# Kernel tuning notes

Measured on AMD Instinct MI355X. Metric: run time of the kernel, lower is better.

The kernel has to match this reference:

```python
import jax, jax.numpy as jnp
import numpy as np

N = 100000
E = 600000
IN_DIM, HID_DIM, OUT_DIM = 128, 64, 3


def setup_inputs() -> dict:
    key = jax.random.key(0)
    ks = jax.random.split(key, 8)
    x = jax.random.normal(ks[0], (N, IN_DIM), dtype=jnp.float32)
    edge_index = jax.random.randint(ks[1], (2, E), 0, N, dtype=jnp.int64)
    # SAGEConv layer 1: lin_l (neighbors, with bias), lin_r (root, no bias)
    s1 = 1.0 / np.sqrt(IN_DIM)
    Wl1 = jax.random.uniform(ks[2], (IN_DIM, HID_DIM), jnp.float32, -s1, s1)
    Wr1 = jax.random.uniform(ks[3], (IN_DIM, HID_DIM), jnp.float32, -s1, s1)
    b1 = jnp.zeros((HID_DIM,), jnp.float32)
    # SAGEConv layer 2
    s2 = 1.0 / np.sqrt(HID_DIM)
    Wl2 = jax.random.uniform(ks[4], (HID_DIM, OUT_DIM), jnp.float32, -s2, s2)
    Wr2 = jax.random.uniform(ks[5], (HID_DIM, OUT_DIM), jnp.float32, -s2, s2)
    b2 = jnp.zeros((OUT_DIM,), jnp.float32)
    return {"x": x, "edge_index": edge_index,
            "Wl1": Wl1, "Wr1": Wr1, "b1": b1,
            "Wl2": Wl2, "Wr2": Wr2, "b2": b2}


def _mean_aggregate(h, src, dst, num_nodes):
    # mean of source-node features over incoming edges per destination node
    summed = jax.ops.segment_sum(h[src], dst, num_segments=num_nodes)  # [N, F]
    cnt = jax.ops.segment_sum(jnp.ones((src.shape[0],), h.dtype), dst,
                              num_segments=num_nodes)
    return summed / jnp.maximum(cnt, 1.0)[:, None]


def _sage_conv(h, src, dst, Wl, Wr, b, num_nodes):
    # PyG SAGEConv (aggr='mean'): lin_l(mean_j x_j) + lin_r(x_i)
    agg = _mean_aggregate(h, src, dst, num_nodes)
    return agg @ Wl + h @ Wr + b


def reference(x, edge_index, Wl1, Wr1, b1, Wl2, Wr2, b2):
    src, dst = edge_index[0], edge_index[1]  # flow: source_to_target
    n = x.shape[0]
    h = jax.nn.relu(_sage_conv(x, src, dst, Wl1, Wr1, b1, n))
    out = _sage_conv(h, src, dst, Wl2, Wr2, b2, n)
    return jax.nn.log_softmax(out, axis=1)
```

## Files before the change

kernel.cpp:

```cpp
#include <hip/hip_runtime.h>
#include <hip/hip_bf16.h>

#define IN_DIM 128
#define HID 64
#define SCAN_B 1024
#define WSTR 136
#define PB 768

using half8 = __attribute__((ext_vector_type(8))) _Float16;
using half2v = __attribute__((ext_vector_type(2))) _Float16;
using f32x4 = __attribute__((ext_vector_type(4))) float;

__global__ __launch_bounds__(256) void init_kernel(
    const float* __restrict__ Wl, const float* __restrict__ Wr,
    _Float16* __restrict__ wcatT, int4* __restrict__ deg4, int n4) {
  const int i = blockIdx.x * 256 + threadIdx.x;
  if (i < 16384) {
    const int col = i >> 7;
    const int k = i & 127;
    const float v = (col < 64) ? Wl[k * HID + col] : Wr[k * HID + col - 64];
    wcatT[col * 128 + k] = (_Float16)v;
  }
  if (i < n4) deg4[i] = (int4){0, 0, 0, 0};
}

__global__ __launch_bounds__(256) void proj1_count_kernel(
    const float* __restrict__ x, const _Float16* __restrict__ wcatT,
    _Float16* __restrict__ xW, _Float16* __restrict__ xWr, int N, int ntiles,
    const int* __restrict__ ei, int* __restrict__ deg_i,
    int* __restrict__ eoff, int E) {
  const int tx = threadIdx.x;
  if (blockIdx.x >= PB) {
    const int nb = gridDim.x - PB;
    for (int e = (blockIdx.x - PB) * 256 + tx; e < E; e += nb * 256)
      eoff[e] = atomicAdd(&deg_i[ei[E + e]], 1);
    return;
  }
  __shared__ _Float16 wsT[128][WSTR];

#pragma unroll
  for (int it = 0; it < 8; ++it) {
    const int e8 = it * 256 + tx;
    const int col = e8 >> 4;
    const int k8 = (e8 & 15) * 8;
    *(half8*)&wsT[col][k8] = *(const half8*)&wcatT[col * 128 + k8];
  }

  const int lane = tx & 63;
  const int wv = tx >> 6;
  const int lrow = lane & 15;
  const int g = lane >> 4;
  const float4* x4 = (const float4*)x;

  __syncthreads();

#pragma unroll 1
  for (int tile = blockIdx.x; tile < ntiles; tile += PB) {
    const int n0 = tile * 64;
    const int row = n0 + wv * 16 + lrow;

    f32x4 acc[8];
#pragma unroll
    for (int ct = 0; ct < 8; ++ct) acc[ct] = (f32x4){0.f, 0.f, 0.f, 0.f};

#pragma unroll
    for (int kt = 0; kt < 4; ++kt) {
      half8 a;
      if (row < N) {
        const float4 u = x4[(size_t)row * 32 + kt * 8 + g * 2];
        const float4 v = x4[(size_t)row * 32 + kt * 8 + g * 2 + 1];
        a[0] = (_Float16)u.x; a[1] = (_Float16)u.y;
        a[2] = (_Float16)u.z; a[3] = (_Float16)u.w;
        a[4] = (_Float16)v.x; a[5] = (_Float16)v.y;
        a[6] = (_Float16)v.z; a[7] = (_Float16)v.w;
      } else {
        a = (half8){0, 0, 0, 0, 0, 0, 0, 0};
      }
#pragma unroll
      for (int ct = 0; ct < 8; ++ct) {
        const half8 b = *(const half8*)&wsT[ct * 16 + lrow][kt * 32 + g * 8];
        acc[ct] =
            __builtin_amdgcn_mfma_f32_16x16x32_f16(a, b, acc[ct], 0, 0, 0);
      }
    }

#pragma unroll
    for (int ct = 0; ct < 8; ++ct) {
      const int col = ct * 16 + lrow;
#pragma unroll
      for (int reg = 0; reg < 4; ++reg) {
        const int nn = n0 + wv * 16 + g * 4 + reg;
        if (nn < N) {
          if (col < 64)
            xW[(size_t)nn * HID + col] = (_Float16)acc[ct][reg];
          else
            xWr[(size_t)nn * HID + col - 64] = (_Float16)acc[ct][reg];
        }
      }
    }
  }
}

__global__ __launch_bounds__(SCAN_B) void scan1_kernel(
    const int* __restrict__ in, int* __restrict__ incl, int* __restrict__ bsum,
    int n) {
  __shared__ int s[SCAN_B];
  const int t = threadIdx.x;
  const int i = blockIdx.x * SCAN_B + t;
  int v = (i < n) ? in[i] : 0;
  s[t] = v;
  for (int off = 1; off < SCAN_B; off <<= 1) {
    __syncthreads();
    const int a = (t >= off) ? s[t - off] : 0;
    __syncthreads();
    s[t] += a;
  }
  if (i < n) incl[i] = s[t];
  if (t == SCAN_B - 1) bsum[blockIdx.x] = s[t];
}

__global__ __launch_bounds__(256) void scan23_kernel(
    const int* __restrict__ incl, const int* __restrict__ deg_i,
    const int* __restrict__ bsum, int* __restrict__ row_off, int n) {
  __shared__ int sred[256];
  const int t = threadIdx.x;
  const int chunk = blockIdx.x >> 2;
  sred[t] = (t < chunk) ? bsum[t] : 0;
  __syncthreads();
#pragma unroll
  for (int off = 128; off >= 1; off >>= 1) {
    if (t < off) sred[t] += sred[t + off];
    __syncthreads();
  }
  const int boff = sred[0];
  const int i = blockIdx.x * 256 + t;
  if (i < n) row_off[i] = incl[i] - deg_i[i] + boff;
}

__global__ __launch_bounds__(256) void fill_kernel(
    const int* __restrict__ ei, const int* __restrict__ row_off,
    const int* __restrict__ eoff, int* __restrict__ csr_src, int E) {
  const int e = blockIdx.x * blockDim.x + threadIdx.x;
  if (e < E) {
    const int s = ei[e];
    const int d = ei[E + e];
    atomicExch(&csr_src[row_off[d] + eoff[e]], s);
  }
}

__global__ __launch_bounds__(256) void layer1_kernel(
    const int* __restrict__ row_off, const int* __restrict__ deg_i,
    const int* __restrict__ csr_src, const _Float16* __restrict__ xW,
    const _Float16* __restrict__ xWr, const float* __restrict__ b1,
    const float* __restrict__ Wl2, const float* __restrict__ Wr2,
    float* __restrict__ pl, float* __restrict__ pr, int N, int ntiles) {
  __shared__ _Float16 wlds[16][72];
  __shared__ _Float16 hlds[64][72];
  const int tx = threadIdx.x;
  for (int i = tx; i < 1024; i += 256) {
    const int c = i >> 6;
    const int k = i & 63;
    float v = 0.f;
    if (c < 3) v = Wl2[k * 3 + c];
    else if (c < 6) v = Wr2[k * 3 + (c - 3)];
    wlds[c][k] = (_Float16)v;
  }
  const int lane = tx & 63;
  const int wv = tx >> 6;
  const int lrow = lane & 15;
  const int g = lane >> 4;
  const int half = lane >> 5;
  const int c2 = lane & 31;
  const float2 bb2 = *(const float2*)&b1[2 * c2];
  const half2v* xW2 = (const half2v*)xW;
  const half2v* xWr2 = (const half2v*)xWr;
  __syncthreads();

#pragma unroll 1
  for (int tile = blockIdx.x; tile < ntiles; tile += gridDim.x) {
    const int base = tile * 64;
#pragma unroll 1
    for (int p = 0; p < 8; ++p) {
      const int nl = 2 * p + half;
      const int myN = base + wv * 16 + nl;
      float a0x = 0.f, a0y = 0.f, a1x = 0.f, a1y = 0.f;
      float a2x = 0.f, a2y = 0.f, a3x = 0.f, a3y = 0.f;
      int start = 0, dg = 0;
      if (myN < N) {
        start = row_off[myN];
        dg = deg_i[myN];
      }
      int r = 0;
      for (; r + 3 < dg; r += 4) {
        const int s0 = csr_src[start + r];
        const int s1 = csr_src[start + r + 1];
        const int s2 = csr_src[start + r + 2];
        const int s3 = csr_src[start + r + 3];
        const half2v v0 = xW2[(size_t)s0 * 32 + c2];
        const half2v v1 = xW2[(size_t)s1 * 32 + c2];
        const half2v v2 = xW2[(size_t)s2 * 32 + c2];
        const half2v v3 = xW2[(size_t)s3 * 32 + c2];
        a0x += (float)v0.x; a0y += (float)v0.y;
        a1x += (float)v1.x; a1y += (float)v1.y;
        a2x += (float)v2.x; a2y += (float)v2.y;
        a3x += (float)v3.x; a3y += (float)v3.y;
      }
      for (; r < dg; ++r) {
        const half2v v0 = xW2[(size_t)csr_src[start + r] * 32 + c2];
        a0x += (float)v0.x; a0y += (float)v0.y;
      }
      const float dinv = 1.0f / fmaxf((float)dg, 1.0f);
      half2v wr = {0, 0};
      if (myN < N) wr = xWr2[(size_t)myN * 32 + c2];
      const float hx =
          fmaxf(((a0x + a1x) + (a2x + a3x)) * dinv + (float)wr.x + bb2.x, 0.f);
      const float hy =
          fmaxf(((a0y + a1y) + (a2y + a3y)) * dinv + (float)wr.y + bb2.y, 0.f);
      half2v hv;
      hv.x = (_Float16)hx;
      hv.y = (_Float16)hy;
      *(half2v*)&hlds[wv * 16 + nl][2 * c2] = hv;
    }
    __syncthreads();
    f32x4 acc = (f32x4){0.f, 0.f, 0.f, 0.f};
#pragma unroll
    for (int kt = 0; kt < 2; ++kt) {
      const half8 a = *(const half8*)&hlds[wv * 16 + lrow][kt * 32 + g * 8];
      const half8 b = *(const half8*)&wlds[lrow][kt * 32 + g * 8];
      acc = __builtin_amdgcn_mfma_f32_16x16x32_f16(a, b, acc, 0, 0, 0);
    }
    if (lrow < 6) {
#pragma unroll
      for (int reg = 0; reg < 4; ++reg) {
        const int n = base + wv * 16 + g * 4 + reg;
        if (n < N) {
          if (lrow < 3)
            pl[(size_t)n * 3 + lrow] = acc[reg];
          else
            pr[(size_t)n * 3 + lrow - 3] = acc[reg];
        }
      }
    }
    __syncthreads();
  }
}

__global__ __launch_bounds__(256) void final_kernel(
    const int* __restrict__ row_off, const int* __restrict__ deg_i,
    const int* __restrict__ csr_src, const float* __restrict__ pl,
    const float* __restrict__ pr, const float* __restrict__ b2,
    float* __restrict__ out, int N) {
  const int stride = gridDim.x * blockDim.x;
  const float b20 = b2[0], b21 = b2[1], b22 = b2[2];
  for (int n = blockIdx.x * blockDim.x + threadIdx.x; n < N; n += stride) {
    const int start = row_off[n];
    const int dg = deg_i[n];
    float s0 = 0.f, s1 = 0.f, s2 = 0.f;
    float t0 = 0.f, t1 = 0.f, t2 = 0.f;
    int r = 0;
    for (; r + 1 < dg; r += 2) {
      const int sa = csr_src[start + r];
      const int sb = csr_src[start + r + 1];
      s0 += pl[(size_t)sa * 3 + 0];
      s1 += pl[(size_t)sa * 3 + 1];
      s2 += pl[(size_t)sa * 3 + 2];
      t0 += pl[(size_t)sb * 3 + 0];
      t1 += pl[(size_t)sb * 3 + 1];
      t2 += pl[(size_t)sb * 3 + 2];
    }
    if (r < dg) {
      const int sa = csr_src[start + r];
      s0 += pl[(size_t)sa * 3 + 0];
      s1 += pl[(size_t)sa * 3 + 1];
      s2 += pl[(size_t)sa * 3 + 2];
    }
    const float dinv = 1.0f / fmaxf((float)dg, 1.0f);
    const float v0 = (s0 + t0) * dinv + pr[(size_t)n * 3 + 0] + b20;
    const float v1 = (s1 + t1) * dinv + pr[(size_t)n * 3 + 1] + b21;
    const float v2 = (s2 + t2) * dinv + pr[(size_t)n * 3 + 2] + b22;
    const float m = fmaxf(fmaxf(v0, v1), v2);
    const float e0 = __expf(v0 - m), e1 = __expf(v1 - m), e2 = __expf(v2 - m);
    const float lse = __logf(e0 + e1 + e2);
    out[(size_t)n * 3 + 0] = v0 - m - lse;
    out[(size_t)n * 3 + 1] = v1 - m - lse;
    out[(size_t)n * 3 + 2] = v2 - m - lse;
  }
}

extern "C" void kernel_launch(void* const* d_in, const int* in_sizes, int n_in,
                              void* d_out, int out_size, void* d_ws,
                              size_t ws_size, hipStream_t stream) {
  const float* x = (const float*)d_in[0];
  const int* ei = (const int*)d_in[1];
  const float* Wl1 = (const float*)d_in[2];
  const float* Wr1 = (const float*)d_in[3];
  const float* b1 = (const float*)d_in[4];
  const float* Wl2 = (const float*)d_in[5];
  const float* Wr2 = (const float*)d_in[6];
  const float* b2 = (const float*)d_in[7];
  float* out = (float*)d_out;

  const int N = in_sizes[0] / IN_DIM;
  const int E = in_sizes[1] / 2;
  const int nb1 = (N + SCAN_B - 1) / SCAN_B;
  const int ntiles = (N + 63) / 64;

  int* wsI = (int*)d_ws;
  int* deg_i = wsI;
  int* row_off = deg_i + N;
  int* incl = row_off + N;
  int* bsum = incl + N;
  int* eoff = bsum + SCAN_B;
  int* csr_src = eoff + E;
  _Float16* wcatT = (_Float16*)(csr_src + E);
  _Float16* xW = wcatT + 128 * 128;
  _Float16* xWr = xW + (size_t)N * HID;
  float* pl = (float*)(xWr + (size_t)N * HID);
  float* pr = pl + (size_t)N * 3;

  const int n4 = (N + 3) / 4;
  const int initg = (max(n4, 16384) + 255) / 256;
  init_kernel<<<initg, 256, 0, stream>>>(Wl1, Wr1, wcatT, (int4*)deg_i, n4);
  proj1_count_kernel<<<PB + 512, 256, 0, stream>>>(x, wcatT, xW, xWr, N,
                                                   ntiles, ei, deg_i, eoff, E);
  scan1_kernel<<<nb1, SCAN_B, 0, stream>>>(deg_i, incl, bsum, N);
  scan23_kernel<<<(N + 255) / 256, 256, 0, stream>>>(incl, deg_i, bsum,
                                                     row_off, N);
  fill_kernel<<<(E + 255) / 256, 256, 0, stream>>>(ei, row_off, eoff, csr_src,
                                                   E);
  layer1_kernel<<<ntiles, 256, 0, stream>>>(row_off, deg_i, csr_src, xW, xWr,
                                            b1, Wl2, Wr2, pl, pr, N, ntiles);
  final_kernel<<<(N + 255) / 256, 256, 0, stream>>>(row_off, deg_i, csr_src,
                                                    pl, pr, b2, out, N);
}
```

Baseline: 116.6 us.

## Launch one block per tile and read weights from global instead of LDS

The projection kernel drops its persistent-block loop (768 blocks striding over tiles) and instead launches one block per 64-row tile. It also stops staging the transposed weight matrix in shared memory and loads the B fragments straight from global/L2. This removes the LDS staging and barrier, lowers LDS use so more blocks can be resident, and gives more parallelism. In exchange every block re-reads the 32KB weight matrix through the cache hierarchy, and the grid now has about 2000 blocks.

```diff
diff --git a/kernel.cpp b/kernel.cpp
--- a/kernel.cpp
+++ b/kernel.cpp
@@ -4,8 +4,7 @@
 #define IN_DIM 128
 #define HID 64
 #define SCAN_B 1024
-#define WSTR 136
-#define PB 768
+#define CB 512
 
 using half8 = __attribute__((ext_vector_type(8))) _Float16;
 using half2v = __attribute__((ext_vector_type(2))) _Float16;
@@ -30,72 +29,57 @@
     const int* __restrict__ ei, int* __restrict__ deg_i,
     int* __restrict__ eoff, int E) {
   const int tx = threadIdx.x;
-  if (blockIdx.x >= PB) {
-    const int nb = gridDim.x - PB;
-    for (int e = (blockIdx.x - PB) * 256 + tx; e < E; e += nb * 256)
+  if (blockIdx.x >= ntiles) {
+    const int nb = gridDim.x - ntiles;
+    for (int e = (blockIdx.x - ntiles) * 256 + tx; e < E; e += nb * 256)
       eoff[e] = atomicAdd(&deg_i[ei[E + e]], 1);
     return;
   }
-  __shared__ _Float16 wsT[128][WSTR];
-
-#pragma unroll
-  for (int it = 0; it < 8; ++it) {
-    const int e8 = it * 256 + tx;
-    const int col = e8 >> 4;
-    const int k8 = (e8 & 15) * 8;
-    *(half8*)&wsT[col][k8] = *(const half8*)&wcatT[col * 128 + k8];
-  }
-
   const int lane = tx & 63;
   const int wv = tx >> 6;
   const int lrow = lane & 15;
   const int g = lane >> 4;
   const float4* x4 = (const float4*)x;
 
-  __syncthreads();
-
-#pragma unroll 1
-  for (int tile = blockIdx.x; tile < ntiles; tile += PB) {
-    const int n0 = tile * 64;
-    const int row = n0 + wv * 16 + lrow;
-
-    f32x4 acc[8];
-#pragma unroll
-    for (int ct = 0; ct < 8; ++ct) acc[ct] = (f32x4){0.f, 0.f, 0.f, 0.f};
-
-#pragma unroll
-    for (int kt = 0; kt < 4; ++kt) {
-      half8 a;
-      if (row < N) {
-        const float4 u = x4[(size_t)row * 32 + kt * 8 + g * 2];
-        const float4 v = x4[(size_t)row * 32 + kt * 8 + g * 2 + 1];
-        a[0] = (_Float16)u.x; a[1] = (_Float16)u.y;
-        a[2] = (_Float16)u.z; a[3] = (_Float16)u.w;
-        a[4] = (_Float16)v.x; a[5] = (_Float16)v.y;
-        a[6] = (_Float16)v.z; a[7] = (_Float16)v.w;
-      } else {
-        a = (half8){0, 0, 0, 0, 0, 0, 0, 0};
-      }
-#pragma unroll
-      for (int ct = 0; ct < 8; ++ct) {
-        const half8 b = *(const half8*)&wsT[ct * 16 + lrow][kt * 32 + g * 8];
-        acc[ct] =
-            __builtin_amdgcn_mfma_f32_16x16x32_f16(a, b, acc[ct], 0, 0, 0);
-      }
-    }
-
+  const int n0 = blockIdx.x * 64;
+  const int row = n0 + wv * 16 + lrow;
+
+  f32x4 acc[8];
+#pragma unroll
+  for (int ct = 0; ct < 8; ++ct) acc[ct] = (f32x4){0.f, 0.f, 0.f, 0.f};
+
+#pragma unroll
+  for (int kt = 0; kt < 4; ++kt) {
+    half8 a;
+    if (row < N) {
+      const float4 u = x4[(size_t)row * 32 + kt * 8 + g * 2];
+      const float4 v = x4[(size_t)row * 32 + kt * 8 + g * 2 + 1];
+      a[0] = (_Float16)u.x; a[1] = (_Float16)u.y;
+      a[2] = (_Float16)u.z; a[3] = (_Float16)u.w;
+      a[4] = (_Float16)v.x; a[5] = (_Float16)v.y;
+      a[6] = (_Float16)v.z; a[7] = (_Float16)v.w;
+    } else {
+      a = (half8){0, 0, 0, 0, 0, 0, 0, 0};
+    }
 #pragma unroll
     for (int ct = 0; ct < 8; ++ct) {
-      const int col = ct * 16 + lrow;
-#pragma unroll
-      for (int reg = 0; reg < 4; ++reg) {
-        const int nn = n0 + wv * 16 + g * 4 + reg;
-        if (nn < N) {
-          if (col < 64)
-            xW[(size_t)nn * HID + col] = (_Float16)acc[ct][reg];
-          else
-            xWr[(size_t)nn * HID + col - 64] = (_Float16)acc[ct][reg];
-        }
+      const half8 b =
+          *(const half8*)&wcatT[(ct * 16 + lrow) * 128 + kt * 32 + g * 8];
+      acc[ct] = __builtin_amdgcn_mfma_f32_16x16x32_f16(a, b, acc[ct], 0, 0, 0);
+    }
+  }
+
+#pragma unroll
+  for (int ct = 0; ct < 8; ++ct) {
+    const int col = ct * 16 + lrow;
+#pragma unroll
+    for (int reg = 0; reg < 4; ++reg) {
+      const int nn = n0 + wv * 16 + g * 4 + reg;
+      if (nn < N) {
+        if (col < 64)
+          xW[(size_t)nn * HID + col] = (_Float16)acc[ct][reg];
+        else
+          xWr[(size_t)nn * HID + col - 64] = (_Float16)acc[ct][reg];
       }
     }
   }
@@ -321,8 +305,8 @@
   const int n4 = (N + 3) / 4;
   const int initg = (max(n4, 16384) + 255) / 256;
   init_kernel<<<initg, 256, 0, stream>>>(Wl1, Wr1, wcatT, (int4*)deg_i, n4);
-  proj1_count_kernel<<<PB + 512, 256, 0, stream>>>(x, wcatT, xW, xWr, N,
-                                                   ntiles, ei, deg_i, eoff, E);
+  proj1_count_kernel<<<ntiles + CB, 256, 0, stream>>>(
+      x, wcatT, xW, xWr, N, ntiles, ei, deg_i, eoff, E);
   scan1_kernel<<<nb1, SCAN_B, 0, stream>>>(deg_i, incl, bsum, N);
   scan23_kernel<<<(N + 255) / 256, 256, 0, stream>>>(incl, deg_i, bsum,
                                                      row_off, N);
```

Measured after the change: 141.3 us. 21.2% more time.
